# Performance work log

Measured on AMD Instinct MI355X. Metric: run time of the kernel, lower is better.

## Reference

```python
import jax, jax.numpy as jnp
import numpy as np

B, CIN, COUT, H, W = 8, 64, 64, 128, 128
HEADS, CR = 4, 32  # reduced_ch = CIN // 2
N = H * W


def build_grid_edges(P, Pw):
    """Directed 4-neighborhood grid edges + self loops, matching build_grid_edge_index."""
    src, dst = [], []
    for i in range(P):
        for j in range(Pw):
            u = i * Pw + j
            if i - 1 >= 0:
                src.append(u); dst.append((i - 1) * Pw + j)
            if i + 1 < P:
                src.append(u); dst.append((i + 1) * Pw + j)
            if j - 1 >= 0:
                src.append(u); dst.append(i * Pw + j - 1)
            if j + 1 < Pw:
                src.append(u); dst.append(i * Pw + j + 1)
            src.append(u); dst.append(u)
    return np.asarray(src, np.int32), np.asarray(dst, np.int32)


def setup_inputs() -> dict:
    key = jax.random.key(0)
    ks = jax.random.split(key, 6)
    src_np, dst_np = build_grid_edges(H, W)
    return {
        "x": jax.random.normal(ks[0], (B, CIN, H, W), jnp.float32),
        "w_reduce": jax.random.normal(ks[1], (CR, CIN), jnp.float32) * (1.0 / np.sqrt(CIN)),
        "w_lin": jax.random.normal(ks[2], (HEADS * CR, CR), jnp.float32) * (1.0 / np.sqrt(CR)),
        "att_src": jax.random.normal(ks[3], (HEADS, CR), jnp.float32) * 0.1,
        "att_dst": jax.random.normal(ks[4], (HEADS, CR), jnp.float32) * 0.1,
        "b_gat": jnp.zeros((CR,), jnp.float32),
        "w_restore": jax.random.normal(ks[5], (COUT, CR), jnp.float32) * (1.0 / np.sqrt(CR)),
        "bn_gamma": jnp.ones((COUT,), jnp.float32),
        "bn_beta": jnp.zeros((COUT,), jnp.float32),
        "src": jnp.asarray(src_np),
        "dst": jnp.asarray(dst_np),
    }


def reference(x, w_reduce, w_lin, att_src, att_dst, b_gat, w_restore, bn_gamma, bn_beta, src, dst):
    b, cin, h, w = x.shape
    heads, cr = att_src.shape
    n = h * w
    res = x  # residual is Identity since input_channels == output_channels

    xr = jnp.einsum('oc,bchw->bohw', w_reduce, x)          # 1x1 reduce conv
    nodes = xr.transpose(0, 2, 3, 1).reshape(b, n, cr)      # [B, N, Cr]

    def gat(nd):
        # PyG GATConv: lin -> per-edge attention -> segment softmax -> scatter sum -> head mean + bias
        hfeat = (nd @ w_lin.T).reshape(n, heads, cr)        # [N, H, Cr]
        a_s = jnp.sum(hfeat * att_src, axis=-1)             # [N, H]
        a_d = jnp.sum(hfeat * att_dst, axis=-1)             # [N, H]
        e = a_s[src] + a_d[dst]                             # [E, H]
        e = jnp.where(e > 0, e, 0.2 * e)                    # leaky_relu(0.2)
        emax = jax.ops.segment_max(e, dst, num_segments=n)  # softmax over incoming edges
        ex = jnp.exp(e - emax[dst])
        denom = jax.ops.segment_sum(ex, dst, num_segments=n)
        alpha = ex / denom[dst]                             # [E, H]
        msg = alpha[:, :, None] * hfeat[src]                # [E, H, Cr]
        agg = jax.ops.segment_sum(msg, dst, num_segments=n) # [N, H, Cr]
        return agg.mean(axis=1) + b_gat                     # concat=False -> head mean, + bias

    g = jax.vmap(gat)(nodes)                                # [B, N, Cr]
    g = g.reshape(b, h, w, cr).transpose(0, 3, 1, 2)

    out = jnp.einsum('oc,bchw->bohw', w_restore, g) + res   # 1x1 restore conv + residual

    # BatchNorm2d (training mode: batch statistics, biased variance)
    mean = out.mean(axis=(0, 2, 3), keepdims=True)
    var = out.var(axis=(0, 2, 3), keepdims=True)
    out = (out - mean) / jnp.sqrt(var + 1e-5)
    out = out * bn_gamma[None, :, None, None] + bn_beta[None, :, None, None]
    return jax.nn.relu(out)
```

## Files before the change

### kernel.cpp

```cpp
#include <hip/hip_runtime.h>

#define NN 16384
#define CINC 64

__global__ void gat_k0(const float* __restrict__ w_restore,
                       const float* __restrict__ b_gat,
                       const float* __restrict__ w_reduce,
                       const float* __restrict__ w_lin,
                       const float* __restrict__ att_src,
                       const float* __restrict__ att_dst,
                       float* __restrict__ rb, float* __restrict__ wredT,
                       float* __restrict__ S, float* __restrict__ D) {
    int t = threadIdx.x;
    if (t < 128) {
        int h = t >> 5, k = t & 31;
        float s = 0.f, d = 0.f;
        for (int c = 0; c < 32; ++c) {
            float wl = w_lin[(h * 32 + c) * 32 + k];
            s += att_src[h * 32 + c] * wl;
            d += att_dst[h * 32 + c] * wl;
        }
        S[t] = s; D[t] = d;
    } else if (t < 192) {
        int o = t - 128;
        float r = 0.f;
        for (int c = 0; c < 32; ++c) r += w_restore[o * 32 + c] * b_gat[c];
        rb[o] = r;
    }
    for (int idx = t; idx < 2048; idx += 256) {
        int k = idx & 31, c = idx >> 5;
        wredT[c * 32 + k] = w_reduce[k * 64 + c];
    }
}

__global__ __launch_bounds__(256) void gat_k1(
        const float* __restrict__ x, const float* __restrict__ wredT,
        const float* __restrict__ S, const float* __restrict__ D,
        float* __restrict__ red_g, float* __restrict__ as_ws,
        float* __restrict__ ad_ws) {
    __shared__ float xs[4096];
    __shared__ float red_lds[32][64];

    int tid = threadIdx.x;
    int s = blockIdx.x;
    int b = s >> 8;
    int v0 = (s & 255) << 6;

    const float* xb = x + (size_t)b * CINC * NN + v0;
    for (int idx = tid; idx < 4096; idx += 256) {
        int c = idx >> 6, nd = idx & 63;
        xs[idx] = xb[(size_t)c * NN + nd];
    }
    __syncthreads();

    int nd = tid & 63;
    int wv = __builtin_amdgcn_readfirstlane(tid >> 6);

    {
        float a0 = 0.f, a1 = 0.f, a2 = 0.f, a3 = 0.f,
              a4 = 0.f, a5 = 0.f, a6 = 0.f, a7 = 0.f;
        const float* wt = wredT + wv * 8;
#pragma unroll 4
        for (int c = 0; c < 64; ++c) {
            float xc = xs[c * 64 + nd];
            const float* w = wt + c * 32;
            a0 = fmaf(w[0], xc, a0);
            a1 = fmaf(w[1], xc, a1);
            a2 = fmaf(w[2], xc, a2);
            a3 = fmaf(w[3], xc, a3);
            a4 = fmaf(w[4], xc, a4);
            a5 = fmaf(w[5], xc, a5);
            a6 = fmaf(w[6], xc, a6);
            a7 = fmaf(w[7], xc, a7);
        }
        int k0 = wv * 8;
        float* rg = red_g + (size_t)b * 32 * NN + v0 + nd;
        red_lds[k0 + 0][nd] = a0; rg[(size_t)(k0 + 0) * NN] = a0;
        red_lds[k0 + 1][nd] = a1; rg[(size_t)(k0 + 1) * NN] = a1;
        red_lds[k0 + 2][nd] = a2; rg[(size_t)(k0 + 2) * NN] = a2;
        red_lds[k0 + 3][nd] = a3; rg[(size_t)(k0 + 3) * NN] = a3;
        red_lds[k0 + 4][nd] = a4; rg[(size_t)(k0 + 4) * NN] = a4;
        red_lds[k0 + 5][nd] = a5; rg[(size_t)(k0 + 5) * NN] = a5;
        red_lds[k0 + 6][nd] = a6; rg[(size_t)(k0 + 6) * NN] = a6;
        red_lds[k0 + 7][nd] = a7; rg[(size_t)(k0 + 7) * NN] = a7;
    }
    __syncthreads();

    {
        float rv[32];
#pragma unroll
        for (int k = 0; k < 32; ++k) rv[k] = red_lds[k][nd];
        const float* sp = S + wv * 32;
        const float* dp = D + wv * 32;
        float pas = 0.f, pad_ = 0.f;
#pragma unroll
        for (int k = 0; k < 32; ++k) {
            pas  = fmaf(sp[k], rv[k], pas);
            pad_ = fmaf(dp[k], rv[k], pad_);
        }
        as_ws[((size_t)b * 4 + wv) * NN + v0 + nd] = pas;
        ad_ws[((size_t)b * 4 + wv) * NN + v0 + nd] = pad_;
    }
}

__global__ __launch_bounds__(256) void gat_k2(
        const float* __restrict__ x, const float* __restrict__ w_lin,
        const float* __restrict__ w_restore, const float* __restrict__ rb,
        const float* __restrict__ red_g, const float* __restrict__ as_ws,
        const float* __restrict__ ad_ws, float* __restrict__ outp,
        float* __restrict__ part) {
    __shared__ float gp[4][8][64];
    __shared__ float gout[32][64];
    __shared__ float stat_lds[128];

    int tid = threadIdx.x;
    int s = blockIdx.x;
    int b = s >> 8;
    int v0 = (s & 255) << 6;
    int nd = tid & 63;
    int h = __builtin_amdgcn_readfirstlane(tid >> 6);
    int v = v0 + nd;
    int i = v >> 7, j = v & 127;

    int un0 = v;
    int un1 = i > 0   ? v - 128 : v;
    int un2 = i < 127 ? v + 128 : v;
    int un3 = j > 0   ? v - 1   : v;
    int un4 = j < 127 ? v + 1   : v;

    float a0, a1, a2, a3, a4;
    {
        const float* asp = as_ws + ((size_t)b * 4 + h) * NN;
        float adv = ad_ws[((size_t)b * 4 + h) * NN + v];
        float e0 = asp[un0] + adv, e1 = asp[un1] + adv, e2 = asp[un2] + adv,
              e3 = asp[un3] + adv, e4 = asp[un4] + adv;
        e0 = e0 > 0.f ? e0 : 0.2f * e0;
        e1 = e1 > 0.f ? e1 : 0.2f * e1;
        e2 = e2 > 0.f ? e2 : 0.2f * e2;
        e3 = e3 > 0.f ? e3 : 0.2f * e3;
        e4 = e4 > 0.f ? e4 : 0.2f * e4;
        e1 += i > 0   ? 0.f : -1e30f;
        e2 += i < 127 ? 0.f : -1e30f;
        e3 += j > 0   ? 0.f : -1e30f;
        e4 += j < 127 ? 0.f : -1e30f;
        float m = fmaxf(fmaxf(fmaxf(e0, e1), fmaxf(e2, e3)), e4);
        e0 = __expf(e0 - m); e1 = __expf(e1 - m); e2 = __expf(e2 - m);
        e3 = __expf(e3 - m); e4 = __expf(e4 - m);
        float sc = 0.25f / (e0 + e1 + e2 + e3 + e4);
        a0 = e0 * sc; a1 = e1 * sc; a2 = e2 * sc; a3 = e3 * sc; a4 = e4 * sc;
    }

    float gpart[32];
#pragma unroll
    for (int c = 0; c < 32; ++c) gpart[c] = 0.f;

    const float* rp = red_g + (size_t)b * 32 * NN;
    const float* wl_h = w_lin + (size_t)h * 32 * 32;
#pragma unroll 1
    for (int kc = 0; kc < 4; ++kc) {
        float racc8[8];
#pragma unroll
        for (int i8 = 0; i8 < 8; ++i8) {
            const float* rk = rp + (size_t)(kc * 8 + i8) * NN;
            racc8[i8] = a0 * rk[un0] + a1 * rk[un1] + a2 * rk[un2] +
                        a3 * rk[un3] + a4 * rk[un4];
        }
        const float* wk = wl_h + kc * 8;
#pragma unroll
        for (int c = 0; c < 32; ++c) {
            gpart[c] += wk[c * 32 + 0] * racc8[0] + wk[c * 32 + 1] * racc8[1] +
                        wk[c * 32 + 2] * racc8[2] + wk[c * 32 + 3] * racc8[3] +
                        wk[c * 32 + 4] * racc8[4] + wk[c * 32 + 5] * racc8[5] +
                        wk[c * 32 + 6] * racc8[6] + wk[c * 32 + 7] * racc8[7];
        }
    }

#pragma unroll
    for (int q = 0; q < 4; ++q) {
#pragma unroll
        for (int cq = 0; cq < 8; ++cq) gp[h][cq][nd] = gpart[q * 8 + cq];
        __syncthreads();
#pragma unroll
        for (int t2 = 0; t2 < 2; ++t2) {
            int cq = h * 2 + t2;
            gout[q * 8 + cq][nd] = gp[0][cq][nd] + gp[1][cq][nd] +
                                   gp[2][cq][nd] + gp[3][cq][nd];
        }
        __syncthreads();
    }

    {
        float gv[32];
#pragma unroll
        for (int c = 0; c < 32; ++c) gv[c] = gout[c][nd];
        const float* xb = x + (size_t)b * CINC * NN + v0 + nd;
        float* ob = outp + (size_t)b * CINC * NN + v0 + nd;
        const float* wr_h = w_restore + (size_t)h * 16 * 32;
#pragma unroll 2
        for (int o16 = 0; o16 < 16; ++o16) {
            int o = h * 16 + o16;
            const float* wr = wr_h + o16 * 32;
            float acc = rb[o];
#pragma unroll
            for (int c = 0; c < 32; ++c)
                acc = fmaf(wr[c], gv[c], acc);
            acc += xb[(size_t)o * NN];
            ob[(size_t)o * NN] = acc;
            float r1 = acc, r2 = acc * acc;
#pragma unroll
            for (int off = 32; off > 0; off >>= 1) {
                r1 += __shfl_xor(r1, off, 64);
                r2 += __shfl_xor(r2, off, 64);
            }
            if (nd == 0) { stat_lds[o] = r1; stat_lds[64 + o] = r2; }
        }
    }
    __syncthreads();
    if (tid < 128) part[(size_t)s * 128 + tid] = stat_lds[tid];
}

__global__ __launch_bounds__(256) void gat_k2b(
        const float* __restrict__ part, float* __restrict__ stats) {
    __shared__ float red[4];
    int jj = blockIdx.x;
    int tid = threadIdx.x;
    float acc = 0.f;
    for (int s = tid; s < 2048; s += 256) acc += part[(size_t)s * 128 + jj];
#pragma unroll
    for (int off = 32; off > 0; off >>= 1) acc += __shfl_xor(acc, off, 64);
    int wv = tid >> 6, lane = tid & 63;
    if (lane == 0) red[wv] = acc;
    __syncthreads();
    if (tid == 0) stats[jj] = red[0] + red[1] + red[2] + red[3];
}

__global__ __launch_bounds__(256) void gat_k3(
        float* __restrict__ out, const float* __restrict__ stats,
        const float* __restrict__ gamma, const float* __restrict__ beta) {
    int f = blockIdx.x * 256 + threadIdx.x;
    int e = f * 4;
    int c = (e >> 14) & 63;
    const float cnt_inv = 1.f / 131072.f;
    float mean = stats[c] * cnt_inv;
    float var = stats[64 + c] * cnt_inv - mean * mean;
    float inv = rsqrtf(var + 1e-5f);
    float sc = gamma[c] * inv;
    float sh = beta[c] - mean * sc;
    float4 vv = reinterpret_cast<float4*>(out)[f];
    vv.x = fmaxf(vv.x * sc + sh, 0.f);
    vv.y = fmaxf(vv.y * sc + sh, 0.f);
    vv.z = fmaxf(vv.z * sc + sh, 0.f);
    vv.w = fmaxf(vv.w * sc + sh, 0.f);
    reinterpret_cast<float4*>(out)[f] = vv;
}

extern "C" void kernel_launch(void* const* d_in, const int* in_sizes, int n_in,
                              void* d_out, int out_size, void* d_ws, size_t ws_size,
                              hipStream_t stream) {
    const float* x         = (const float*)d_in[0];
    const float* w_reduce  = (const float*)d_in[1];
    const float* w_lin     = (const float*)d_in[2];
    const float* att_src   = (const float*)d_in[3];
    const float* att_dst   = (const float*)d_in[4];
    const float* b_gat     = (const float*)d_in[5];
    const float* w_restore = (const float*)d_in[6];
    const float* bn_gamma  = (const float*)d_in[7];
    const float* bn_beta   = (const float*)d_in[8];

    float* ws     = (float*)d_ws;
    float* red_g  = ws;
    float* as_ws  = red_g + 4194304;
    float* ad_ws  = as_ws + 524288;
    float* Sf     = ad_ws + 524288;
    float* Df     = Sf + 128;
    float* rbf    = Df + 128;
    float* wredT  = rbf + 64;
    float* stats  = wredT + 2048;
    float* part   = stats + 128;

    gat_k0<<<1, 256, 0, stream>>>(w_restore, b_gat, w_reduce, w_lin,
                                  att_src, att_dst, rbf, wredT, Sf, Df);
    gat_k1<<<2048, 256, 0, stream>>>(x, wredT, Sf, Df, red_g, as_ws, ad_ws);
    gat_k2<<<2048, 256, 0, stream>>>(x, w_lin, w_restore, rbf, red_g,
                                     as_ws, ad_ws, (float*)d_out, part);
    gat_k2b<<<128, 256, 0, stream>>>(part, stats);
    gat_k3<<<8192, 256, 0, stream>>>((float*)d_out, stats, bn_gamma, bn_beta);
}
```

Measured before the change: 102.7 us.

## Split GAT aggregation across waves by input channel instead of by head

Each wave now computes attention coefficients for all four heads and handles an 8-channel slice of the reduced features, instead of one head over all 32 channels. Each wave therefore gathers the neighbour values for only its own 8 channels, cutting redundant global gathers of red_g by four, and combines them with w_lin for every head. The cost is four times the softmax and exponential work per thread, more registers for the coefficients of all heads, and more scalar w_lin loads per channel chunk.

```diff
diff --git a/kernel.cpp b/kernel.cpp
--- a/kernel.cpp
+++ b/kernel.cpp
@@ -118,7 +118,7 @@
     int b = s >> 8;
     int v0 = (s & 255) << 6;
     int nd = tid & 63;
-    int h = __builtin_amdgcn_readfirstlane(tid >> 6);
+    int wv = __builtin_amdgcn_readfirstlane(tid >> 6);
     int v = v0 + nd;
     int i = v >> 7, j = v & 127;
 
@@ -128,8 +128,9 @@
     int un3 = j > 0   ? v - 1   : v;
     int un4 = j < 127 ? v + 1   : v;
 
-    float a0, a1, a2, a3, a4;
-    {
+    float al[4][5];
+#pragma unroll
+    for (int h = 0; h < 4; ++h) {
         const float* asp = as_ws + ((size_t)b * 4 + h) * NN;
         float adv = ad_ws[((size_t)b * 4 + h) * NN + v];
         float e0 = asp[un0] + adv, e1 = asp[un1] + adv, e2 = asp[un2] + adv,
@@ -147,42 +148,50 @@
         e0 = __expf(e0 - m); e1 = __expf(e1 - m); e2 = __expf(e2 - m);
         e3 = __expf(e3 - m); e4 = __expf(e4 - m);
         float sc = 0.25f / (e0 + e1 + e2 + e3 + e4);
-        a0 = e0 * sc; a1 = e1 * sc; a2 = e2 * sc; a3 = e3 * sc; a4 = e4 * sc;
+        al[h][0] = e0 * sc; al[h][1] = e1 * sc; al[h][2] = e2 * sc;
+        al[h][3] = e3 * sc; al[h][4] = e4 * sc;
     }
 
     float gpart[32];
 #pragma unroll
     for (int c = 0; c < 32; ++c) gpart[c] = 0.f;
 
-    const float* rp = red_g + (size_t)b * 32 * NN;
-    const float* wl_h = w_lin + (size_t)h * 32 * 32;
+    const float* rp = red_g + (size_t)b * 32 * NN + (size_t)(wv * 8) * NN;
+    const float* wl = w_lin;
 #pragma unroll 1
     for (int kc = 0; kc < 4; ++kc) {
-        float racc8[8];
-#pragma unroll
-        for (int i8 = 0; i8 < 8; ++i8) {
-            const float* rk = rp + (size_t)(kc * 8 + i8) * NN;
-            racc8[i8] = a0 * rk[un0] + a1 * rk[un1] + a2 * rk[un2] +
-                        a3 * rk[un3] + a4 * rk[un4];
-        }
-        const float* wk = wl_h + kc * 8;
+        const float* rk0 = rp + (size_t)(kc * 2) * NN;
+        const float* rk1 = rk0 + NN;
+        float t00 = rk0[un0], t01 = rk0[un1], t02 = rk0[un2],
+              t03 = rk0[un3], t04 = rk0[un4];
+        float t10 = rk1[un0], t11 = rk1[un1], t12 = rk1[un2],
+              t13 = rk1[un3], t14 = rk1[un4];
+        float r0[4], r1[4];
+#pragma unroll
+        for (int h = 0; h < 4; ++h) {
+            r0[h] = al[h][0] * t00 + al[h][1] * t01 + al[h][2] * t02 +
+                    al[h][3] * t03 + al[h][4] * t04;
+            r1[h] = al[h][0] * t10 + al[h][1] * t11 + al[h][2] * t12 +
+                    al[h][3] * t13 + al[h][4] * t14;
+        }
 #pragma unroll
         for (int c = 0; c < 32; ++c) {
-            gpart[c] += wk[c * 32 + 0] * racc8[0] + wk[c * 32 + 1] * racc8[1] +
-                        wk[c * 32 + 2] * racc8[2] + wk[c * 32 + 3] * racc8[3] +
-                        wk[c * 32 + 4] * racc8[4] + wk[c * 32 + 5] * racc8[5] +
-                        wk[c * 32 + 6] * racc8[6] + wk[c * 32 + 7] * racc8[7];
+#pragma unroll
+            for (int h = 0; h < 4; ++h) {
+                const float* wk = wl + (h * 32 + c) * 32 + wv * 8 + kc * 2;
+                gpart[c] += wk[0] * r0[h] + wk[1] * r1[h];
+            }
         }
     }
 
 #pragma unroll
     for (int q = 0; q < 4; ++q) {
 #pragma unroll
-        for (int cq = 0; cq < 8; ++cq) gp[h][cq][nd] = gpart[q * 8 + cq];
+        for (int cq = 0; cq < 8; ++cq) gp[wv][cq][nd] = gpart[q * 8 + cq];
         __syncthreads();
 #pragma unroll
         for (int t2 = 0; t2 < 2; ++t2) {
-            int cq = h * 2 + t2;
+            int cq = wv * 2 + t2;
             gout[q * 8 + cq][nd] = gp[0][cq][nd] + gp[1][cq][nd] +
                                    gp[2][cq][nd] + gp[3][cq][nd];
         }
@@ -195,10 +204,10 @@
         for (int c = 0; c < 32; ++c) gv[c] = gout[c][nd];
         const float* xb = x + (size_t)b * CINC * NN + v0 + nd;
         float* ob = outp + (size_t)b * CINC * NN + v0 + nd;
-        const float* wr_h = w_restore + (size_t)h * 16 * 32;
+        const float* wr_h = w_restore + (size_t)wv * 16 * 32;
 #pragma unroll 2
         for (int o16 = 0; o16 < 16; ++o16) {
-            int o = h * 16 + o16;
+            int o = wv * 16 + o16;
             const float* wr = wr_h + o16 * 32;
             float acc = rb[o];
 #pragma unroll
```

Measured after the change: 103.0 us. Within noise of the previous version (+0.3%).
